# Performance work log

Hardware: AMD Instinct MI355X
Metric: run time of the kernel (lower is better)

## Reference

```python
import jax, jax.numpy as jnp
import numpy as np

N, E, G = 10000, 160000, 64
NODE_DIM, HID = 128, 256


def _edge_conv(x, src, dst, w1, b1, w2, b2):
    # gather endpoints: x_i = target features, x_j = source features (PyG source_to_target)
    x_i = x[dst]                              # [E, C]
    x_j = x[src]                              # [E, C]
    m = jnp.concatenate([x_i, x_j - x_i], axis=-1)  # [E, 2C]
    m = jax.nn.relu(m @ w1 + b1) @ w2 + b2          # [E, H]
    out = jax.ops.segment_max(m, dst, num_segments=N)  # scatter-max per target node
    return out  # nodes with no in-edges get -inf; subsequent relu maps them to 0 (matches PyG fill 0 + relu)


def setup_inputs() -> dict:
    key = jax.random.key(0)
    ks = jax.random.split(key, 20)
    x = jax.random.normal(ks[0], (N, NODE_DIM), dtype=jnp.float32)
    edge_index = jax.random.randint(ks[1], (2, E), 0, N)
    batch = jnp.sort(jax.random.randint(ks[2], (N,), 0, G))
    s = 0.05
    inp = {"x": x, "edge_index": edge_index, "batch": batch}
    dims = [(2 * NODE_DIM, HID), (2 * HID, HID), (2 * HID, HID)]
    for li, (din, dout) in enumerate(dims):
        inp[f"c{li}_w1"] = jax.random.normal(ks[3 + 4 * li], (din, dout), jnp.float32) * s
        inp[f"c{li}_b1"] = jnp.zeros((dout,), jnp.float32)
        inp[f"c{li}_w2"] = jax.random.normal(ks[4 + 4 * li], (dout, dout), jnp.float32) * s
        inp[f"c{li}_b2"] = jnp.zeros((dout,), jnp.float32)
    inp["cl_w1"] = jax.random.normal(ks[15], (2 * HID, HID), jnp.float32) * s
    inp["cl_b1"] = jnp.zeros((HID,), jnp.float32)
    inp["cl_w2"] = jax.random.normal(ks[16], (HID, 64), jnp.float32) * s
    inp["cl_b2"] = jnp.zeros((64,), jnp.float32)
    inp["cl_w3"] = jax.random.normal(ks[17], (64, 1), jnp.float32) * s
    inp["cl_b3"] = jnp.zeros((1,), jnp.float32)
    return inp


def reference(x, edge_index, batch,
              c0_w1, c0_b1, c0_w2, c0_b2,
              c1_w1, c1_b1, c1_w2, c1_b2,
              c2_w1, c2_b1, c2_w2, c2_b2,
              cl_w1, cl_b1, cl_w2, cl_b2, cl_w3, cl_b3):
    src, dst = edge_index[0], edge_index[1]
    for (w1, b1, w2, b2) in [(c0_w1, c0_b1, c0_w2, c0_b2),
                             (c1_w1, c1_b1, c1_w2, c1_b2),
                             (c2_w1, c2_b1, c2_w2, c2_b2)]:
        x = jax.nn.relu(_edge_conv(x, src, dst, w1, b1, w2, b2))
    # global mean / max pool per graph
    sums = jax.ops.segment_sum(x, batch, num_segments=G)
    counts = jax.ops.segment_sum(jnp.ones((x.shape[0], 1), x.dtype), batch, num_segments=G)
    x_mean = sums / jnp.maximum(counts, 1.0)
    x_max = jax.ops.segment_max(x, batch, num_segments=G)
    x_max = jnp.where(counts > 0, x_max, 0.0)
    h = jnp.concatenate([x_mean, x_max], axis=1)  # [G, 2H]
    h = jax.nn.relu(h @ cl_w1 + cl_b1)            # dropout is eval-mode identity
    h = jax.nn.relu(h @ cl_w2 + cl_b2)
    out = (h @ cl_w3 + cl_b3).squeeze(-1)         # [G]
    return out
```

## Files before the change

kernel.cpp:

```cpp
#include <hip/hip_runtime.h>


#define NN 10000
#define NE 160000
#define NG 64
#define NP 10048
#define EB 64

typedef __attribute__((ext_vector_type(8))) _Float16 f16x8;
typedef __attribute__((ext_vector_type(4))) _Float16 f16x4;
typedef __attribute__((ext_vector_type(4))) float f32x4;

__global__ void hist_kernel(const int* __restrict__ dstI, int* __restrict__ hist) {
    int i = blockIdx.x * blockDim.x + threadIdx.x;
    if (i < NE) atomicAdd(&hist[dstI[i]], 1);
}

__global__ void scan_kernel(const int* __restrict__ hist, int* __restrict__ cursor) {
    __shared__ int sums[256];
    const int t = threadIdx.x;
    const int per = (NN + 255) / 256;
    const int lo = t * per, hi = (lo + per < NN) ? lo + per : NN;
    int s = 0;
    for (int i = lo; i < hi; ++i) s += hist[i];
    sums[t] = s;
    __syncthreads();
    for (int ofs = 1; ofs < 256; ofs <<= 1) {
        int add = (t >= ofs) ? sums[t - ofs] : 0;
        __syncthreads();
        sums[t] += add;
        __syncthreads();
    }
    int run = sums[t] - s;
    for (int i = lo; i < hi; ++i) {
        int h = hist[i];
        cursor[i] = run;
        run += h;
    }
}

__global__ void scatter_kernel(const int* __restrict__ srcI, const int* __restrict__ dstI,
                               int* __restrict__ cursor,
                               int* __restrict__ se2, int* __restrict__ de2) {
    int i = blockIdx.x * blockDim.x + threadIdx.x;
    if (i < NE) {
        int d = dstI[i];
        int p = atomicAdd(&cursor[d], 1);
        se2[p] = srcI[i];
        de2[p] = d;
    }
}

__global__ void prep_weights(const float* __restrict__ w1, const float* __restrict__ w2, int C,
                             _Float16* __restrict__ WcT, _Float16* __restrict__ w2T) {
    int total1 = 512 * C;
    int total = total1 + 256 * 256;
    for (int i = blockIdx.x * blockDim.x + threadIdx.x; i < total; i += gridDim.x * blockDim.x) {
        if (i < total1) {
            int n = i / C, k = i - n * C;
            float v = (n < 256) ? (w1[k * 256 + n] - w1[(C + k) * 256 + n])
                                : w1[(C + k) * 256 + (n - 256)];
            WcT[n * C + k] = (_Float16)v;
        } else {
            int j = i - total1;
            int n = j >> 8, k = j & 255;
            w2T[n * 256 + k] = (_Float16)w2[k * 256 + n];
        }
    }
}

template <int C>
__global__ void conv_rows(const float* __restrict__ src, _Float16* __restrict__ xh) {
    const int total4 = NP * C / 4;
    const int c4 = C / 4;
    for (int i4 = blockIdx.x * blockDim.x + threadIdx.x; i4 < total4; i4 += gridDim.x * blockDim.x) {
        const int row = i4 / c4;
        f16x4 o;
        if (row < NN) {
            float4 v = ((const float4*)src)[i4];
            o[0] = (_Float16)v.x; o[1] = (_Float16)v.y;
            o[2] = (_Float16)v.z; o[3] = (_Float16)v.w;
        } else {
            o[0] = o[1] = o[2] = o[3] = (_Float16)0.f;
        }
        ((f16x4*)xh)[i4] = o;
    }
}

template <int C>
__global__ __launch_bounds__(256) void node_gemm(
    const _Float16* __restrict__ xh, const _Float16* __restrict__ WT,
    const float* __restrict__ b1, float* __restrict__ Af, _Float16* __restrict__ Bh) {
    const int wave = threadIdx.x >> 6, lane = threadIdx.x & 63;
    const int lrow = lane & 15, lk = (lane >> 4) * 8;
    const int r0 = blockIdx.x * 64;
    const int c0 = blockIdx.y * 128 + wave * 32;

    f32x4 acc[4][2] = {};
#pragma unroll
    for (int kk = 0; kk < C; kk += 32) {
        f16x8 ah[4];
#pragma unroll
        for (int m = 0; m < 4; ++m)
            ah[m] = *(const f16x8*)(xh + (size_t)(r0 + m * 16 + lrow) * C + kk + lk);
#pragma unroll
        for (int t = 0; t < 2; ++t) {
            f16x8 bh = *(const f16x8*)(WT + (size_t)(c0 + t * 16 + lrow) * C + kk + lk);
#pragma unroll
            for (int m = 0; m < 4; ++m)
                acc[m][t] = __builtin_amdgcn_mfma_f32_16x16x32_f16(ah[m], bh, acc[m][t], 0, 0, 0);
        }
    }
    if (blockIdx.y < 2) {
#pragma unroll
        for (int t = 0; t < 2; ++t) {
            const int col = c0 + t * 16 + lrow;
            const float bias = b1[col];
#pragma unroll
            for (int m = 0; m < 4; ++m)
#pragma unroll
                for (int j = 0; j < 4; ++j) {
                    const int row = r0 + m * 16 + (lane >> 4) * 4 + j;
                    Af[(size_t)row * 256 + col] = acc[m][t][j] + bias;
                }
        }
    } else {
#pragma unroll
        for (int t = 0; t < 2; ++t) {
            const int col = c0 - 256 + t * 16 + lrow;
#pragma unroll
            for (int m = 0; m < 4; ++m)
#pragma unroll
                for (int j = 0; j < 4; ++j) {
                    const int row = r0 + m * 16 + (lane >> 4) * 4 + j;
                    Bh[(size_t)row * 256 + col] = (_Float16)acc[m][t][j];
                }
        }
    }
}

__global__ __launch_bounds__(256, 4) void edge_gemm(
    const float* __restrict__ Af, const _Float16* __restrict__ Bh,
    const int* __restrict__ se2, const int* __restrict__ de2,
    const _Float16* __restrict__ w2T,
    const float* __restrict__ b2, float* __restrict__ y) {
    __shared__ _Float16 hh[EB * 256];
    const int tid = threadIdx.x;
    const int wave = tid >> 6, lane = tid & 63;

    const int orig = blockIdx.x;
    const int xcd = orig & 7, pos = orig >> 3;
    const int q = 2500 >> 3, r = 2500 & 7;
    const int bid = (xcd < r ? xcd * (q + 1) : r * (q + 1) + (xcd - r) * q) + pos;
    const int e0 = bid * EB;
    const int ew = wave * 16;

    int se[16], de[16];
#pragma unroll
    for (int i = 0; i < 16; ++i) {
        se[i] = se2[e0 + ew + i];
        de[i] = de2[e0 + ew + i];
    }
#pragma unroll
    for (int b = 0; b < 2; ++b) {
        float4 av[8];
        f16x4 bv[8];
#pragma unroll
        for (int i = 0; i < 8; ++i) {
            const int el = b * 8 + i;
            bv[i] = *(const f16x4*)(Bh + (size_t)se[el] * 256 + lane * 4);
            av[i] = *(const float4*)(Af + (size_t)de[el] * 256 + lane * 4);
        }
#pragma unroll
        for (int i = 0; i < 8; ++i) {
            const int el = b * 8 + i;
            const int row = (el >> 2) * 16 + wave * 4 + (el & 3);
            f16x4 vh;
            vh[0] = (_Float16)fmaxf(av[i].x + (float)bv[i][0], 0.f);
            vh[1] = (_Float16)fmaxf(av[i].y + (float)bv[i][1], 0.f);
            vh[2] = (_Float16)fmaxf(av[i].z + (float)bv[i][2], 0.f);
            vh[3] = (_Float16)fmaxf(av[i].w + (float)bv[i][3], 0.f);
            const int idx = (row * 256 + lane * 4) ^ ((row & 7) << 3);
            *(f16x4*)(&hh[idx]) = vh;
        }
    }
    __syncthreads();

    const int lrow = lane & 15, lk = (lane >> 4) * 8;
    const _Float16* wbase = w2T + (size_t)(wave * 64 + lrow) * 256 + lk;

    f32x4 acc[4][4] = {};
    for (int kk = 0; kk < 256; kk += 32) {
        f16x8 ah[4];
#pragma unroll
        for (int m = 0; m < 4; ++m) {
            const int row = m * 16 + lrow;
            const int idx = (row * 256 + kk + lk) ^ ((row & 7) << 3);
            ah[m] = *(const f16x8*)(&hh[idx]);
        }
#pragma unroll
        for (int t = 0; t < 4; ++t) {
            f16x8 bh = *(const f16x8*)(wbase + (size_t)(t * 16) * 256 + kk);
#pragma unroll
            for (int m = 0; m < 4; ++m)
                acc[m][t] = __builtin_amdgcn_mfma_f32_16x16x32_f16(ah[m], bh, acc[m][t], 0, 0, 0);
        }
    }

    const int g = lane >> 4;
    int d[16];
#pragma unroll
    for (int k = 0; k < 16; ++k) d[k] = de2[e0 + g * 16 + k];
#pragma unroll
    for (int t = 0; t < 4; ++t) {
        const int col = wave * 64 + t * 16 + lrow;
        const float bias = b2[col];
        float run = acc[0][t][0] + bias;
        int dp = d[0];
#pragma unroll
        for (int k = 1; k < 16; ++k) {
            const float v = acc[k >> 2][t][k & 3] + bias;
            if (d[k] == dp) {
                run = fmaxf(run, v);
            } else {
                if (run > 0.f) atomicMax((int*)(y + (size_t)dp * 256 + col), __float_as_int(run));
                run = v;
                dp = d[k];
            }
        }
        if (run > 0.f) atomicMax((int*)(y + (size_t)dp * 256 + col), __float_as_int(run));
    }
}

__global__ void pool_kernel(const float* __restrict__ y, const int* __restrict__ batch,
                            float* __restrict__ pooled) {
    const int g = blockIdx.x;
    __shared__ int slo, shi;
    if (threadIdx.x == 0) {
        int lo = 0, hi = NN;
        while (lo < hi) { int m = (lo + hi) >> 1; if (batch[m] < g) lo = m + 1; else hi = m; }
        slo = lo;
        int lo2 = lo, hi2 = NN;
        while (lo2 < hi2) { int m = (lo2 + hi2) >> 1; if (batch[m] < g + 1) lo2 = m + 1; else hi2 = m; }
        shi = lo2;
    }
    __syncthreads();
    const int lo = slo, hi = shi, c = threadIdx.x;
    float s0 = 0.f, s1 = 0.f, s2 = 0.f, s3 = 0.f;
    float m0 = 0.f, m1 = 0.f, m2 = 0.f, m3 = 0.f;
    int n = lo;
    for (; n + 4 <= hi; n += 4) {
        float v0 = y[(size_t)(n + 0) * 256 + c];
        float v1 = y[(size_t)(n + 1) * 256 + c];
        float v2 = y[(size_t)(n + 2) * 256 + c];
        float v3 = y[(size_t)(n + 3) * 256 + c];
        s0 += v0; s1 += v1; s2 += v2; s3 += v3;
        m0 = fmaxf(m0, v0); m1 = fmaxf(m1, v1); m2 = fmaxf(m2, v2); m3 = fmaxf(m3, v3);
    }
    for (; n < hi; ++n) {
        float v = y[(size_t)n * 256 + c];
        s0 += v; m0 = fmaxf(m0, v);
    }
    const float s = (s0 + s1) + (s2 + s3);
    const float mx = fmaxf(fmaxf(m0, m1), fmaxf(m2, m3));
    const int cnt = hi - lo;
    pooled[g * 512 + c] = cnt ? s / (float)cnt : 0.f;
    pooled[g * 512 + 256 + c] = cnt ? mx : 0.f;
}

__global__ void classifier(const float* __restrict__ pooled,
                           const float* __restrict__ w1, const float* __restrict__ b1,
                           const float* __restrict__ w2, const float* __restrict__ b2,
                           const float* __restrict__ w3, const float* __restrict__ b3,
                           float* __restrict__ out) {
    const int g = blockIdx.x;
    __shared__ float ph[512];
    __shared__ float o1[256];
    __shared__ float o2[64];
    const int t = threadIdx.x;
    ph[t] = pooled[g * 512 + t];
    ph[t + 256] = pooled[g * 512 + 256 + t];
    __syncthreads();
    float s = 0.f;
    for (int k = 0; k < 512; ++k) s += ph[k] * w1[k * 256 + t];
    o1[t] = fmaxf(s + b1[t], 0.f);
    __syncthreads();
    if (t < 64) {
        float s2 = 0.f;
        for (int k = 0; k < 256; ++k) s2 += o1[k] * w2[k * 64 + t];
        o2[t] = fmaxf(s2 + b2[t], 0.f);
    }
    __syncthreads();
    if (t < 64) {
        float v = o2[t] * w3[t];
        for (int off = 32; off; off >>= 1) v += __shfl_down(v, off);
        if (t == 0) out[g] = v + b3[0];
    }
}

extern "C" void kernel_launch(void* const* d_in, const int* in_sizes, int n_in,
                              void* d_out, int out_size, void* d_ws, size_t ws_size,
                              hipStream_t stream) {
    (void)in_sizes; (void)n_in; (void)out_size; (void)ws_size;
    const float* x0 = (const float*)d_in[0];
    const int* eidx = (const int*)d_in[1];
    const int* batch = (const int*)d_in[2];
    const int* srcI = eidx;
    const int* dstI = eidx + NE;

    char* ws = (char*)d_ws;
    size_t off = 0;
    auto alloc = [&](size_t bytes) -> void* {
        void* p = ws + off;
        off += (bytes + 255) & ~(size_t)255;
        return p;
    };
    _Float16* xh = (_Float16*)alloc((size_t)NP * 256 * 2);
    float* Af = (float*)alloc((size_t)NP * 256 * 4);
    _Float16* Bh = (_Float16*)alloc((size_t)NP * 256 * 2);
    float* y  = (float*)alloc((size_t)NP * 256 * 4);
    _Float16* WcT = (_Float16*)alloc(512 * 256 * 2);
    _Float16* w2T = (_Float16*)alloc(256 * 256 * 2);
    float* pooled = (float*)alloc(64 * 512 * 4);
    int* hist = (int*)alloc(NN * 4);
    int* se2 = (int*)alloc(NE * 4);
    int* de2 = (int*)alloc(NE * 4);

    const float* lw[3][4] = {
        {(const float*)d_in[3],  (const float*)d_in[4],  (const float*)d_in[5],  (const float*)d_in[6]},
        {(const float*)d_in[7],  (const float*)d_in[8],  (const float*)d_in[9],  (const float*)d_in[10]},
        {(const float*)d_in[11], (const float*)d_in[12], (const float*)d_in[13], (const float*)d_in[14]},
    };

    hipMemsetAsync(hist, 0, NN * 4, stream);
    hist_kernel<<<dim3((NE + 255) / 256), dim3(256), 0, stream>>>(dstI, hist);
    scan_kernel<<<dim3(1), dim3(256), 0, stream>>>(hist, hist);
    scatter_kernel<<<dim3((NE + 255) / 256), dim3(256), 0, stream>>>(srcI, dstI, hist, se2, de2);

    conv_rows<128><<<dim3(1024), dim3(256), 0, stream>>>(x0, xh);

    for (int l = 0; l < 3; ++l) {
        const int C = (l == 0) ? 128 : 256;
        prep_weights<<<dim3(256), dim3(256), 0, stream>>>(lw[l][0], lw[l][2], C, WcT, w2T);
        if (C == 128)
            node_gemm<128><<<dim3(NP / 64, 4), dim3(256), 0, stream>>>(xh, WcT, lw[l][1], Af, Bh);
        else
            node_gemm<256><<<dim3(NP / 64, 4), dim3(256), 0, stream>>>(xh, WcT, lw[l][1], Af, Bh);
        hipMemsetAsync(y, 0, (size_t)NP * 256 * 4, stream);
        edge_gemm<<<dim3(NE / EB), dim3(256), 0, stream>>>(Af, Bh, se2, de2, w2T, lw[l][3], y);
        if (l < 2)
            conv_rows<256><<<dim3(1024), dim3(256), 0, stream>>>(y, xh);
    }

    pool_kernel<<<dim3(NG), dim3(256), 0, stream>>>(y, batch, pooled);
    classifier<<<dim3(NG), dim3(256), 0, stream>>>(pooled,
        (const float*)d_in[15], (const float*)d_in[16],
        (const float*)d_in[17], (const float*)d_in[18],
        (const float*)d_in[19], (const float*)d_in[20], (float*)d_out);
}
```

Baseline: 358.1 us.

## Use 8 waves in edge GEMM, widen node GEMM tiles, prefetch weights

The edge GEMM now runs 512 threads (8 waves) per 64-edge block. Each wave gathers 8 edges and computes a 64x32 output slice instead of 64x64, with a software-prefetched double buffer for the W2 fragments. The bias add is moved after the per-segment max, so it runs once per atomic instead of once per element. The node GEMM doubles each wave's column tile to 64 and halves grid.y, trading more accumulator registers for fewer reloads of the A rows. The aim is more latency hiding for the gather and MFMA work, at the risk of lower occupancy under the 512-thread launch bound.

```diff
diff --git a/kernel.cpp b/kernel.cpp
--- a/kernel.cpp
+++ b/kernel.cpp
@@ -94,9 +94,9 @@
     const int wave = threadIdx.x >> 6, lane = threadIdx.x & 63;
     const int lrow = lane & 15, lk = (lane >> 4) * 8;
     const int r0 = blockIdx.x * 64;
-    const int c0 = blockIdx.y * 128 + wave * 32;
-
-    f32x4 acc[4][2] = {};
+    const int c0 = blockIdx.y * 256 + wave * 64;
+
+    f32x4 acc[4][4] = {};
 #pragma unroll
     for (int kk = 0; kk < C; kk += 32) {
         f16x8 ah[4];
@@ -104,16 +104,16 @@
         for (int m = 0; m < 4; ++m)
             ah[m] = *(const f16x8*)(xh + (size_t)(r0 + m * 16 + lrow) * C + kk + lk);
 #pragma unroll
-        for (int t = 0; t < 2; ++t) {
+        for (int t = 0; t < 4; ++t) {
             f16x8 bh = *(const f16x8*)(WT + (size_t)(c0 + t * 16 + lrow) * C + kk + lk);
 #pragma unroll
             for (int m = 0; m < 4; ++m)
                 acc[m][t] = __builtin_amdgcn_mfma_f32_16x16x32_f16(ah[m], bh, acc[m][t], 0, 0, 0);
         }
     }
-    if (blockIdx.y < 2) {
-#pragma unroll
-        for (int t = 0; t < 2; ++t) {
+    if (blockIdx.y == 0) {
+#pragma unroll
+        for (int t = 0; t < 4; ++t) {
             const int col = c0 + t * 16 + lrow;
             const float bias = b1[col];
 #pragma unroll
@@ -126,7 +126,7 @@
         }
     } else {
 #pragma unroll
-        for (int t = 0; t < 2; ++t) {
+        for (int t = 0; t < 4; ++t) {
             const int col = c0 - 256 + t * 16 + lrow;
 #pragma unroll
             for (int m = 0; m < 4; ++m)
@@ -139,7 +139,7 @@
     }
 }
 
-__global__ __launch_bounds__(256, 4) void edge_gemm(
+__global__ __launch_bounds__(512, 4) void edge_gemm(
     const float* __restrict__ Af, const _Float16* __restrict__ Bh,
     const int* __restrict__ se2, const int* __restrict__ de2,
     const _Float16* __restrict__ w2T,
@@ -153,28 +153,25 @@
     const int q = 2500 >> 3, r = 2500 & 7;
     const int bid = (xcd < r ? xcd * (q + 1) : r * (q + 1) + (xcd - r) * q) + pos;
     const int e0 = bid * EB;
-    const int ew = wave * 16;
-
-    int se[16], de[16];
-#pragma unroll
-    for (int i = 0; i < 16; ++i) {
-        se[i] = se2[e0 + ew + i];
-        de[i] = de2[e0 + ew + i];
-    }
-#pragma unroll
-    for (int b = 0; b < 2; ++b) {
+
+    {
+        int se[8], de[8];
+#pragma unroll
+        for (int i = 0; i < 8; ++i) {
+            se[i] = se2[e0 + wave * 8 + i];
+            de[i] = de2[e0 + wave * 8 + i];
+        }
         float4 av[8];
         f16x4 bv[8];
 #pragma unroll
         for (int i = 0; i < 8; ++i) {
-            const int el = b * 8 + i;
-            bv[i] = *(const f16x4*)(Bh + (size_t)se[el] * 256 + lane * 4);
-            av[i] = *(const float4*)(Af + (size_t)de[el] * 256 + lane * 4);
+            bv[i] = *(const f16x4*)(Bh + (size_t)se[i] * 256 + lane * 4);
+            av[i] = *(const float4*)(Af + (size_t)de[i] * 256 + lane * 4);
         }
 #pragma unroll
         for (int i = 0; i < 8; ++i) {
-            const int el = b * 8 + i;
-            const int row = (el >> 2) * 16 + wave * 4 + (el & 3);
+            const int el = wave * 8 + i;
+            const int row = ((el >> 2) & 3) * 16 + (el >> 4) * 4 + (el & 3);
             f16x4 vh;
             vh[0] = (_Float16)fmaxf(av[i].x + (float)bv[i][0], 0.f);
             vh[1] = (_Float16)fmaxf(av[i].y + (float)bv[i][1], 0.f);
@@ -187,10 +184,18 @@
     __syncthreads();
 
     const int lrow = lane & 15, lk = (lane >> 4) * 8;
-    const _Float16* wbase = w2T + (size_t)(wave * 64 + lrow) * 256 + lk;
-
-    f32x4 acc[4][4] = {};
+    const _Float16* wbase = w2T + (size_t)(wave * 32 + lrow) * 256 + lk;
+
+    f32x4 acc[4][2] = {};
+    f16x8 bhA[2], bhB[2];
+    bhA[0] = *(const f16x8*)(wbase);
+    bhA[1] = *(const f16x8*)(wbase + 16 * 256);
+#pragma unroll
     for (int kk = 0; kk < 256; kk += 32) {
+        if (kk + 32 < 256) {
+            bhB[0] = *(const f16x8*)(wbase + kk + 32);
+            bhB[1] = *(const f16x8*)(wbase + 16 * 256 + kk + 32);
+        }
         f16x8 ah[4];
 #pragma unroll
         for (int m = 0; m < 4; ++m) {
@@ -199,12 +204,12 @@
             ah[m] = *(const f16x8*)(&hh[idx]);
         }
 #pragma unroll
-        for (int t = 0; t < 4; ++t) {
-            f16x8 bh = *(const f16x8*)(wbase + (size_t)(t * 16) * 256 + kk);
+        for (int t = 0; t < 2; ++t)
 #pragma unroll
             for (int m = 0; m < 4; ++m)
-                acc[m][t] = __builtin_amdgcn_mfma_f32_16x16x32_f16(ah[m], bh, acc[m][t], 0, 0, 0);
-        }
+                acc[m][t] = __builtin_amdgcn_mfma_f32_16x16x32_f16(ah[m], bhA[t], acc[m][t], 0, 0, 0);
+        bhA[0] = bhB[0];
+        bhA[1] = bhB[1];
     }
 
     const int g = lane >> 4;
@@ -212,23 +217,25 @@
 #pragma unroll
     for (int k = 0; k < 16; ++k) d[k] = de2[e0 + g * 16 + k];
 #pragma unroll
-    for (int t = 0; t < 4; ++t) {
-        const int col = wave * 64 + t * 16 + lrow;
+    for (int t = 0; t < 2; ++t) {
+        const int col = wave * 32 + t * 16 + lrow;
         const float bias = b2[col];
-        float run = acc[0][t][0] + bias;
+        float run = acc[0][t][0];
         int dp = d[0];
 #pragma unroll
         for (int k = 1; k < 16; ++k) {
-            const float v = acc[k >> 2][t][k & 3] + bias;
+            const float v = acc[k >> 2][t][k & 3];
             if (d[k] == dp) {
                 run = fmaxf(run, v);
             } else {
-                if (run > 0.f) atomicMax((int*)(y + (size_t)dp * 256 + col), __float_as_int(run));
+                const float o = run + bias;
+                if (o > 0.f) atomicMax((int*)(y + (size_t)dp * 256 + col), __float_as_int(o));
                 run = v;
                 dp = d[k];
             }
         }
-        if (run > 0.f) atomicMax((int*)(y + (size_t)dp * 256 + col), __float_as_int(run));
+        const float o = run + bias;
+        if (o > 0.f) atomicMax((int*)(y + (size_t)dp * 256 + col), __float_as_int(o));
     }
 }
 
@@ -343,11 +350,11 @@
         const int C = (l == 0) ? 128 : 256;
         prep_weights<<<dim3(256), dim3(256), 0, stream>>>(lw[l][0], lw[l][2], C, WcT, w2T);
         if (C == 128)
-            node_gemm<128><<<dim3(NP / 64, 4), dim3(256), 0, stream>>>(xh, WcT, lw[l][1], Af, Bh);
+            node_gemm<128><<<dim3(NP / 64, 2), dim3(256), 0, stream>>>(xh, WcT, lw[l][1], Af, Bh);
         else
-            node_gemm<256><<<dim3(NP / 64, 4), dim3(256), 0, stream>>>(xh, WcT, lw[l][1], Af, Bh);
+            node_gemm<256><<<dim3(NP / 64, 2), dim3(256), 0, stream>>>(xh, WcT, lw[l][1], Af, Bh);
         hipMemsetAsync(y, 0, (size_t)NP * 256 * 4, stream);
-        edge_gemm<<<dim3(NE / EB), dim3(256), 0, stream>>>(Af, Bh, se2, de2, w2T, lw[l][3], y);
+        edge_gemm<<<dim3(NE / EB), dim3(512), 0, stream>>>(Af, Bh, se2, de2, w2T, lw[l][3], y);
         if (l < 2)
             conv_rows<256><<<dim3(1024), dim3(256), 0, stream>>>(y, xh);
     }
```

After: 363.2 us, median of 5. Within noise of the previous version (+1.4%).
